# Kernel tuning notes

Hardware: AMD Instinct MI355X
Metric: run time of the kernel (lower is better)

## Reference

```python
import jax, jax.numpy as jnp
import numpy as np

N_NODES = 50000
N_EDGES = 800000
RATIO = 0.5


def setup_inputs() -> dict:
    key = jax.random.key(0)
    ks = jax.random.split(key, 10)
    x = jax.random.normal(ks[0], (N_NODES, 256), dtype=jnp.float32)
    edge_index = jax.random.randint(ks[1], (2, N_EDGES), 0, N_NODES, dtype=jnp.int32)
    edge_weight = jax.random.uniform(ks[2], (N_EDGES,), dtype=jnp.float32)
    sub_fea = jax.random.normal(ks[3], (1, 128), dtype=jnp.float32)
    W1 = jax.random.normal(ks[4], (256, 96), dtype=jnp.float32) * 0.05
    b1 = jax.random.normal(ks[5], (96,), dtype=jnp.float32) * 0.05
    W2 = jax.random.normal(ks[6], (96, 64), dtype=jnp.float32) * 0.05
    b2 = jax.random.normal(ks[7], (64,), dtype=jnp.float32) * 0.05
    fc_w = jax.random.normal(ks[8], (64, 128), dtype=jnp.float32) * 0.05
    fc_b = jax.random.normal(ks[9], (64,), dtype=jnp.float32) * 0.05
    return {"x": x, "edge_index": edge_index, "edge_weight": edge_weight,
            "sub_fea": sub_fea, "W1": W1, "b1": b1, "W2": W2, "b2": b2,
            "fc_w": fc_w, "fc_b": fc_b}


def reference(x, edge_index, edge_weight, sub_fea, W1, b1, W2, b2, fc_w, fc_b):
    N = x.shape[0]
    src, dst = edge_index[0], edge_index[1]

    def gcn_layer(h, W, b):
        # GraphConvolution: support = h @ W; out = spmm(adj, support) + b
        support = h @ W                              # [N, d_out]
        msgs = support[src] * edge_weight[:, None]   # gather + scale, [E, d_out]
        agg = jax.ops.segment_sum(msgs, dst, num_segments=N)  # scatter-add
        return agg + b

    h = jax.nn.relu(gcn_layer(x, W1, b1))            # [N, nhid]
    h = jax.nn.relu(gcn_layer(h, W2, b2))            # [N, nclass]
    # global_mean_pool(batch=None): mean over all nodes -> [1, nclass]
    pooled = jax.nn.selu(jnp.mean(h, axis=0, keepdims=True))
    # dropout in eval mode: identity
    x_ext = sub_fea @ fc_w.T + fc_b                  # [1, nclass]
    out = pooled + RATIO * x_ext
    return jax.nn.log_softmax(out, axis=1)
```

## Files before the change

### kernel.cpp

```cpp
#include <hip/hip_runtime.h>
#include <hip/hip_bf16.h>

#define N_NODES 50000
#define N_EDGES 800000
#define NBKT ((N_NODES + 127) / 128)
#define BCAP 4096

typedef __attribute__((ext_vector_type(8))) short short8;
typedef __attribute__((ext_vector_type(4))) float float4v;

__device__ __forceinline__ unsigned short f2bf(float f) {
    unsigned u = __float_as_uint(f);
    u += 0x7FFF + ((u >> 16) & 1);
    return (unsigned short)(u >> 16);
}
__device__ __forceinline__ float bf2f(unsigned short u) {
    return __uint_as_float((unsigned)u << 16);
}

__global__ __launch_bounds__(256) void prep_kernel(const float* __restrict__ W1,
                                                   const float* __restrict__ W2,
                                                   unsigned short* __restrict__ Wt1,
                                                   unsigned short* __restrict__ Wt2,
                                                   int* __restrict__ gcnt,
                                                   float* __restrict__ pooled) {
    int i = blockIdx.x * 256 + threadIdx.x;
    if (i < 24576) {
        int n = i >> 8, k = i & 255;
        Wt1[i] = f2bf(W1[k * 96 + n]);
    } else if (i < 30720) {
        int j = i - 24576;
        int n = j / 96, k = j - n * 96;
        Wt2[j] = f2bf(W2[k * 64 + n]);
    } else if (i < 30720 + NBKT) {
        gcnt[i - 30720] = 0;
    } else if (i < 30720 + NBKT + 64) {
        pooled[i - 30720 - NBKT] = 0.f;
    }
}

template <int K, int N, bool IN_BF16>
__global__ __launch_bounds__(256) void gemm_mfma_kernel(const void* __restrict__ src_,
                                                        const unsigned short* __restrict__ Wt,
                                                        unsigned short* __restrict__ outb) {
    constexpr int NF = N / 16;
    constexpr int LDA = 40;
    __shared__ unsigned short a_lds[64 * LDA];
    __shared__ unsigned short b_lds[N * LDA];
    const int tid = threadIdx.x;
    const int lane = tid & 63;
    const int w = tid >> 6;
    const int row0 = blockIdx.x * 64;
    const int fr = lane & 15;
    const int fk = (lane >> 4) * 8;

    float4v acc[NF];
    #pragma unroll
    for (int nn = 0; nn < NF; ++nn) acc[nn] = (float4v){0.f, 0.f, 0.f, 0.f};

    const int srow = tid >> 2;
    const int sko  = (tid & 3) * 8;

    for (int k0 = 0; k0 < K; k0 += 32) {
        {
            int grow = row0 + srow;
            short8 s = (short8){0, 0, 0, 0, 0, 0, 0, 0};
            if (grow < N_NODES) {
                if constexpr (IN_BF16) {
                    const unsigned short* src = (const unsigned short*)src_;
                    s = *reinterpret_cast<const short8*>(&src[(size_t)grow * K + k0 + sko]);
                } else {
                    const float* src = (const float*)src_;
                    const float4* p = reinterpret_cast<const float4*>(&src[(size_t)grow * K + k0 + sko]);
                    float4 v0 = p[0], v1 = p[1];
                    s[0] = (short)f2bf(v0.x); s[1] = (short)f2bf(v0.y);
                    s[2] = (short)f2bf(v0.z); s[3] = (short)f2bf(v0.w);
                    s[4] = (short)f2bf(v1.x); s[5] = (short)f2bf(v1.y);
                    s[6] = (short)f2bf(v1.z); s[7] = (short)f2bf(v1.w);
                }
            }
            *reinterpret_cast<short8*>(&a_lds[srow * LDA + sko]) = s;
        }
        for (int c = tid; c < N * 4; c += 256) {
            int n = c >> 2, ko = (c & 3) * 8;
            short8 s = *reinterpret_cast<const short8*>(&Wt[(size_t)n * K + k0 + ko]);
            *reinterpret_cast<short8*>(&b_lds[n * LDA + ko]) = s;
        }
        __syncthreads();
        short8 af = *reinterpret_cast<short8*>(&a_lds[(w * 16 + fr) * LDA + fk]);
        #pragma unroll
        for (int nn = 0; nn < NF; ++nn) {
            short8 bf = *reinterpret_cast<short8*>(&b_lds[(nn * 16 + fr) * LDA + fk]);
            acc[nn] = __builtin_amdgcn_mfma_f32_16x16x32_bf16(af, bf, acc[nn], 0, 0, 0);
        }
        __syncthreads();
    }
    const int orow_base = row0 + w * 16 + (lane >> 4) * 4;
    const int ocol = lane & 15;
    #pragma unroll
    for (int nn = 0; nn < NF; ++nn) {
        #pragma unroll
        for (int r = 0; r < 4; ++r) {
            int grow = orow_base + r;
            if (grow < N_NODES) outb[(size_t)grow * N + nn * 16 + ocol] = f2bf(acc[nn][r]);
        }
    }
}

__global__ __launch_bounds__(256) void bucket1_kernel(const int* __restrict__ srcv,
                                                      const int* __restrict__ dstv,
                                                      const float* __restrict__ wv,
                                                      int* __restrict__ gcnt,
                                                      int2* __restrict__ scratch) {
    __shared__ int lhist[NBKT];
    __shared__ int gb[NBKT];
    const int t = threadIdx.x;
    for (int i = t; i < NBKT; i += 256) lhist[i] = 0;
    __syncthreads();
    const int base = blockIdx.x * 4096;
    int rank[16], bkt[16], dst[16];
    unsigned pay[16];
    #pragma unroll
    for (int i = 0; i < 16; ++i) {
        int e = base + t + i * 256;
        if (e < N_EDGES) {
            int d = dstv[e];
            dst[i] = d;
            bkt[i] = d >> 7;
            unsigned w15 = __float2uint_rn(wv[e] * 32768.0f);
            if (w15 > 32767u) w15 = 32767u;
            pay[i] = ((unsigned)srcv[e] << 15) | w15;
            rank[i] = atomicAdd(&lhist[bkt[i]], 1);
        } else {
            bkt[i] = -1;
        }
    }
    __syncthreads();
    for (int b = t; b < NBKT; b += 256) {
        int c = lhist[b];
        gb[b] = (c > 0) ? atomicAdd(&gcnt[b], c) : 0;
    }
    __syncthreads();
    #pragma unroll
    for (int i = 0; i < 16; ++i) {
        if (bkt[i] >= 0) {
            int pos = gb[bkt[i]] + rank[i];
            if (pos < BCAP)
                scratch[(size_t)bkt[i] * BCAP + pos] = make_int2(dst[i], (int)pay[i]);
        }
    }
}

__global__ __launch_bounds__(512) void bscan_kernel(const int* __restrict__ gcnt,
                                                    int* __restrict__ bbase,
                                                    int* __restrict__ off) {
    __shared__ int sh[512];
    const int t = threadIdx.x;
    int v = (t < NBKT) ? min(gcnt[t], BCAP) : 0;
    sh[t] = v;
    __syncthreads();
    #pragma unroll
    for (int d = 1; d < 512; d <<= 1) {
        int u = (t >= d) ? sh[t - d] : 0;
        __syncthreads();
        sh[t] += u;
        __syncthreads();
    }
    if (t < NBKT) bbase[t] = sh[t] - v;
    if (t == NBKT - 1) off[N_NODES] = sh[t];
}

__global__ __launch_bounds__(256) void bucket2_kernel(const int2* __restrict__ scratch,
                                                      const int* __restrict__ gcnt,
                                                      const int* __restrict__ bbase,
                                                      int* __restrict__ off,
                                                      unsigned* __restrict__ ewq) {
    __shared__ int dh[128];
    __shared__ int sx[128];
    __shared__ int dcur[128];
    const int t = threadIdx.x;
    const int b = blockIdx.x;
    const int d0 = b << 7;
    const int cnt = min(gcnt[b], BCAP);
    const size_t sbase = (size_t)b * BCAP;
    const int obase = bbase[b];
    if (t < 128) dh[t] = 0;
    __syncthreads();
    for (int i = t; i < cnt; i += 256)
        atomicAdd(&dh[scratch[sbase + i].x & 127], 1);
    __syncthreads();
    int myc = (t < 128) ? dh[t] : 0;
    if (t < 128) sx[t] = myc;
    __syncthreads();
    #pragma unroll
    for (int d = 1; d < 128; d <<= 1) {
        int u = (t < 128 && t >= d) ? sx[t - d] : 0;
        __syncthreads();
        if (t < 128) sx[t] += u;
        __syncthreads();
    }
    if (t < 128) {
        int excl = obase + sx[t] - myc;
        dcur[t] = excl;
        if (d0 + t < N_NODES) off[d0 + t] = excl;
    }
    __syncthreads();
    for (int i = t; i < cnt; i += 256) {
        int2 e = scratch[sbase + i];
        int pos = atomicAdd(&dcur[e.x & 127], 1);
        ewq[pos] = (unsigned)e.y;
    }
}

template <int DIM, bool OUT_BF16>
__global__ __launch_bounds__(256) void gather_agg_kernel(const unsigned short* __restrict__ supb,
                                                         const int* __restrict__ off,
                                                         const unsigned* __restrict__ ewq,
                                                         const float* __restrict__ bias,
                                                         void* __restrict__ outp) {
    const int NQ = DIM / 4;
    const float kInv = 1.0f / 32768.0f;
    unsigned gid = blockIdx.x * 256u + threadIdx.x;
    if (gid >= (unsigned)N_NODES * NQ) return;
    unsigned n = gid / NQ;
    unsigned q = gid - n * NQ;
    const int e0 = off[n], e1 = off[n + 1];
    float4 acc[8];
    #pragma unroll
    for (int i = 0; i < 8; ++i) acc[i] = make_float4(0.f, 0.f, 0.f, 0.f);
    int e = e0;
    for (; e + 8 <= e1; e += 8) {
        unsigned p[8];
        #pragma unroll
        for (int i = 0; i < 8; ++i) p[i] = ewq[e + i];
        ushort4 u[8];
        #pragma unroll
        for (int i = 0; i < 8; ++i)
            u[i] = *reinterpret_cast<const ushort4*>(&supb[(size_t)(p[i] >> 15) * DIM + q * 4]);
        #pragma unroll
        for (int i = 0; i < 8; ++i) {
            float w = (float)(p[i] & 32767u) * kInv;
            acc[i].x += bf2f(u[i].x) * w;
            acc[i].y += bf2f(u[i].y) * w;
            acc[i].z += bf2f(u[i].z) * w;
            acc[i].w += bf2f(u[i].w) * w;
        }
    }
    for (; e < e1; ++e) {
        unsigned p = ewq[e];
        float w = (float)(p & 32767u) * kInv;
        ushort4 u = *reinterpret_cast<const ushort4*>(&supb[(size_t)(p >> 15) * DIM + q * 4]);
        acc[0].x += bf2f(u.x) * w;
        acc[0].y += bf2f(u.y) * w;
        acc[0].z += bf2f(u.z) * w;
        acc[0].w += bf2f(u.w) * w;
    }
    #pragma unroll
    for (int i = 1; i < 8; ++i) {
        acc[0].x += acc[i].x;
        acc[0].y += acc[i].y;
        acc[0].z += acc[i].z;
        acc[0].w += acc[i].w;
    }
    const float4 bb = *reinterpret_cast<const float4*>(&bias[q * 4]);
    float4 r;
    r.x = fmaxf(acc[0].x + bb.x, 0.f);
    r.y = fmaxf(acc[0].y + bb.y, 0.f);
    r.z = fmaxf(acc[0].z + bb.z, 0.f);
    r.w = fmaxf(acc[0].w + bb.w, 0.f);
    if (OUT_BF16) {
        ushort4 o;
        o.x = f2bf(r.x); o.y = f2bf(r.y); o.z = f2bf(r.z); o.w = f2bf(r.w);
        *reinterpret_cast<ushort4*>(&((unsigned short*)outp)[(size_t)n * DIM + q * 4]) = o;
    } else {
        *reinterpret_cast<float4*>(&((float*)outp)[(size_t)n * DIM + q * 4]) = r;
    }
}

__global__ __launch_bounds__(256) void colsum_kernel(const float* __restrict__ h2,
                                                     float* __restrict__ pooled) {
    __shared__ float red[4][64];
    const int t = threadIdx.x;
    const int c = t & 63, r = t >> 6;
    float s = 0.f;
    const int base = blockIdx.x * 256;
    for (int i = r; i < 256; i += 4) {
        int n = base + i;
        if (n < N_NODES) s += h2[(size_t)n * 64 + c];
    }
    red[r][c] = s;
    __syncthreads();
    if (r == 0) {
        float v = red[0][c] + red[1][c] + red[2][c] + red[3][c];
        unsafeAtomicAdd(&pooled[c], v);
    }
}

__global__ void final_kernel(const float* __restrict__ pooled,
                             const float* __restrict__ sub_fea,
                             const float* __restrict__ fc_w,
                             const float* __restrict__ fc_b,
                             float* __restrict__ out) {
    const int c = threadIdx.x;
    float p = pooled[c] * (1.0f / (float)N_NODES);
    const float kScale = 1.0507009873554805f;
    const float kAlpha = 1.6732632423543772f;
    float se = (p > 0.f) ? kScale * p : kScale * kAlpha * (expf(p) - 1.f);
    float xe = fc_b[c];
    for (int k = 0; k < 128; ++k) xe += sub_fea[k] * fc_w[c * 128 + k];
    float v = se + 0.5f * xe;
    float m = v;
    #pragma unroll
    for (int off = 32; off >= 1; off >>= 1) m = fmaxf(m, __shfl_xor(m, off));
    float ex = expf(v - m);
    float ss = ex;
    #pragma unroll
    for (int off = 32; off >= 1; off >>= 1) ss += __shfl_xor(ss, off);
    out[c] = v - m - logf(ss);
}

extern "C" void kernel_launch(void* const* d_in, const int* in_sizes, int n_in,
                              void* d_out, int out_size, void* d_ws, size_t ws_size,
                              hipStream_t stream) {
    const float* x       = (const float*)d_in[0];
    const int*   ei      = (const int*)d_in[1];
    const float* ew      = (const float*)d_in[2];
    const float* sub_fea = (const float*)d_in[3];
    const float* W1      = (const float*)d_in[4];
    const float* b1      = (const float*)d_in[5];
    const float* W2      = (const float*)d_in[6];
    const float* b2      = (const float*)d_in[7];
    const float* fc_w    = (const float*)d_in[8];
    const float* fc_b    = (const float*)d_in[9];
    float* out = (float*)d_out;

    char* base = (char*)d_ws;
    unsigned short* A   = (unsigned short*)(base);
    char*  Bb    = base + 9600000;
    float* pooled = (float*)(base + 22400000);
    int*   off   = (int*)(base + 22400512);
    int*   gcnt  = (int*)(base + 22600704);
    int*   bbase = (int*)(base + 22602752);
    unsigned* ewq = (unsigned*)(base + 22604800);
    int2*  scratch = (int2*)(base + 25804800);
    unsigned short* Wt1 = (unsigned short*)(base + 38617088);
    unsigned short* Wt2 = (unsigned short*)(base + 38666240);

    const int* srcv = ei;
    const int* dstv = ei + N_EDGES;

    prep_kernel<<<122, 256, 0, stream>>>(W1, W2, Wt1, Wt2, gcnt, pooled);

    bucket1_kernel<<<(N_EDGES + 4095) / 4096, 256, 0, stream>>>(srcv, dstv, ew, gcnt, scratch);
    bscan_kernel<<<1, 512, 0, stream>>>(gcnt, bbase, off);
    bucket2_kernel<<<NBKT, 256, 0, stream>>>(scratch, gcnt, bbase, off, ewq);

    gemm_mfma_kernel<256, 96, false><<<(N_NODES + 63) / 64, 256, 0, stream>>>(x, Wt1, A);
    {
        unsigned total = (unsigned)N_NODES * 24;
        gather_agg_kernel<96, true><<<(total + 255) / 256, 256, 0, stream>>>(
            A, off, ewq, b1, Bb);
    }

    gemm_mfma_kernel<96, 64, true><<<(N_NODES + 63) / 64, 256, 0, stream>>>(Bb, Wt2, A);
    {
        unsigned total = (unsigned)N_NODES * 16;
        gather_agg_kernel<64, false><<<(total + 255) / 256, 256, 0, stream>>>(
            A, off, ewq, b2, Bb);
    }

    colsum_kernel<<<(N_NODES + 255) / 256, 256, 0, stream>>>((const float*)Bb, pooled);
    final_kernel<<<1, 64, 0, stream>>>(pooled, sub_fea, fc_w, fc_b, out);
}
```

Before: 141.5 us.

## Fuse edge bucketing with first GEMM, drop scan kernel, store support in FP8

New measurement: 131.7 us. -6.9%, faster.

```diff
diff --git a/kernel.cpp b/kernel.cpp
--- a/kernel.cpp
+++ b/kernel.cpp
@@ -5,6 +5,8 @@
 #define N_EDGES 800000
 #define NBKT ((N_NODES + 127) / 128)
 #define BCAP 4096
+#define NB_B1 ((N_EDGES + 4095) / 4096)
+#define NB_GEMM1 ((N_NODES + 63) / 64)
 
 typedef __attribute__((ext_vector_type(8))) short short8;
 typedef __attribute__((ext_vector_type(4))) float float4v;
@@ -16,6 +18,19 @@
 }
 __device__ __forceinline__ float bf2f(unsigned short u) {
     return __uint_as_float((unsigned)u << 16);
+}
+__device__ __forceinline__ unsigned char f2fp8(float v) {
+    unsigned b = __float_as_uint(v * 0x1p-120f);
+    unsigned s = (b >> 24) & 0x80u;
+    unsigned mag = b & 0x7FFFFFFFu;
+    mag += 0x7FFFFu + ((mag >> 20) & 1u);
+    unsigned code = mag >> 20;
+    if (code > 0x7Eu) code = 0x7Eu;
+    return (unsigned char)(s | code);
+}
+__device__ __forceinline__ float fp82f(unsigned c) {
+    unsigned u = ((c & 0x80u) << 24) | ((c & 0x7Fu) << 20);
+    return __uint_as_float(u) * 0x1p+120f;
 }
 
 __global__ __launch_bounds__(256) void prep_kernel(const float* __restrict__ W1,
@@ -40,17 +55,17 @@
 }
 
 template <int K, int N, bool IN_BF16>
-__global__ __launch_bounds__(256) void gemm_mfma_kernel(const void* __restrict__ src_,
-                                                        const unsigned short* __restrict__ Wt,
-                                                        unsigned short* __restrict__ outb) {
+__device__ __forceinline__ void gemm_body(int bx, const void* __restrict__ src_,
+                                          const unsigned short* __restrict__ Wt,
+                                          unsigned char* __restrict__ outb,
+                                          unsigned short* a_lds,
+                                          unsigned short* b_lds) {
     constexpr int NF = N / 16;
     constexpr int LDA = 40;
-    __shared__ unsigned short a_lds[64 * LDA];
-    __shared__ unsigned short b_lds[N * LDA];
     const int tid = threadIdx.x;
     const int lane = tid & 63;
     const int w = tid >> 6;
-    const int row0 = blockIdx.x * 64;
+    const int row0 = bx * 64;
     const int fr = lane & 15;
     const int fk = (lane >> 4) * 8;
 
@@ -102,88 +117,96 @@
         #pragma unroll
         for (int r = 0; r < 4; ++r) {
             int grow = orow_base + r;
-            if (grow < N_NODES) outb[(size_t)grow * N + nn * 16 + ocol] = f2bf(acc[nn][r]);
-        }
-    }
-}
-
-__global__ __launch_bounds__(256) void bucket1_kernel(const int* __restrict__ srcv,
-                                                      const int* __restrict__ dstv,
-                                                      const float* __restrict__ wv,
-                                                      int* __restrict__ gcnt,
-                                                      int2* __restrict__ scratch) {
+            if (grow < N_NODES) outb[(size_t)grow * N + nn * 16 + ocol] = f2fp8(acc[nn][r]);
+        }
+    }
+}
+
+__global__ __launch_bounds__(256) void mega1_kernel(const int* __restrict__ srcv,
+                                                    const int* __restrict__ dstv,
+                                                    const float* __restrict__ wv,
+                                                    int* __restrict__ gcnt,
+                                                    int2* __restrict__ scratch,
+                                                    const float* __restrict__ x,
+                                                    const unsigned short* __restrict__ Wt1,
+                                                    unsigned char* __restrict__ outA) {
     __shared__ int lhist[NBKT];
     __shared__ int gb[NBKT];
+    __shared__ unsigned short a_lds[64 * 40];
+    __shared__ unsigned short b_lds[96 * 40];
     const int t = threadIdx.x;
-    for (int i = t; i < NBKT; i += 256) lhist[i] = 0;
-    __syncthreads();
-    const int base = blockIdx.x * 4096;
-    int rank[16], bkt[16], dst[16];
-    unsigned pay[16];
-    #pragma unroll
-    for (int i = 0; i < 16; ++i) {
-        int e = base + t + i * 256;
-        if (e < N_EDGES) {
-            int d = dstv[e];
-            dst[i] = d;
-            bkt[i] = d >> 7;
-            unsigned w15 = __float2uint_rn(wv[e] * 32768.0f);
-            if (w15 > 32767u) w15 = 32767u;
-            pay[i] = ((unsigned)srcv[e] << 15) | w15;
-            rank[i] = atomicAdd(&lhist[bkt[i]], 1);
-        } else {
-            bkt[i] = -1;
-        }
-    }
-    __syncthreads();
-    for (int b = t; b < NBKT; b += 256) {
-        int c = lhist[b];
-        gb[b] = (c > 0) ? atomicAdd(&gcnt[b], c) : 0;
-    }
-    __syncthreads();
-    #pragma unroll
-    for (int i = 0; i < 16; ++i) {
-        if (bkt[i] >= 0) {
-            int pos = gb[bkt[i]] + rank[i];
-            if (pos < BCAP)
-                scratch[(size_t)bkt[i] * BCAP + pos] = make_int2(dst[i], (int)pay[i]);
-        }
-    }
-}
-
-__global__ __launch_bounds__(512) void bscan_kernel(const int* __restrict__ gcnt,
-                                                    int* __restrict__ bbase,
-                                                    int* __restrict__ off) {
-    __shared__ int sh[512];
-    const int t = threadIdx.x;
-    int v = (t < NBKT) ? min(gcnt[t], BCAP) : 0;
-    sh[t] = v;
-    __syncthreads();
-    #pragma unroll
-    for (int d = 1; d < 512; d <<= 1) {
-        int u = (t >= d) ? sh[t - d] : 0;
-        __syncthreads();
-        sh[t] += u;
-        __syncthreads();
-    }
-    if (t < NBKT) bbase[t] = sh[t] - v;
-    if (t == NBKT - 1) off[N_NODES] = sh[t];
+    if (blockIdx.x < NB_B1) {
+        for (int i = t; i < NBKT; i += 256) lhist[i] = 0;
+        __syncthreads();
+        const int base = blockIdx.x * 4096;
+        int rank[16], bkt[16], dst[16];
+        unsigned pay[16];
+        #pragma unroll
+        for (int i = 0; i < 16; ++i) {
+            int e = base + t + i * 256;
+            if (e < N_EDGES) {
+                int d = dstv[e];
+                dst[i] = d;
+                bkt[i] = d >> 7;
+                unsigned w15 = __float2uint_rn(wv[e] * 32768.0f);
+                if (w15 > 32767u) w15 = 32767u;
+                pay[i] = ((unsigned)srcv[e] << 15) | w15;
+                rank[i] = atomicAdd(&lhist[bkt[i]], 1);
+            } else {
+                bkt[i] = -1;
+            }
+        }
+        __syncthreads();
+        for (int b = t; b < NBKT; b += 256) {
+            int c = lhist[b];
+            gb[b] = (c > 0) ? atomicAdd(&gcnt[b], c) : 0;
+        }
+        __syncthreads();
+        #pragma unroll
+        for (int i = 0; i < 16; ++i) {
+            if (bkt[i] >= 0) {
+                int pos = gb[bkt[i]] + rank[i];
+                if (pos < BCAP)
+                    scratch[(size_t)bkt[i] * BCAP + pos] = make_int2(dst[i], (int)pay[i]);
+            }
+        }
+    } else {
+        gemm_body<256, 96, false>(blockIdx.x - NB_B1, x, Wt1, outA, a_lds, b_lds);
+    }
+}
+
+__global__ __launch_bounds__(256) void gemm2_kernel(const unsigned short* __restrict__ h1,
+                                                    const unsigned short* __restrict__ Wt2,
+                                                    unsigned char* __restrict__ outA) {
+    __shared__ unsigned short a_lds[64 * 40];
+    __shared__ unsigned short b_lds[64 * 40];
+    gemm_body<96, 64, true>(blockIdx.x, h1, Wt2, outA, a_lds, b_lds);
 }
 
 __global__ __launch_bounds__(256) void bucket2_kernel(const int2* __restrict__ scratch,
                                                       const int* __restrict__ gcnt,
-                                                      const int* __restrict__ bbase,
                                                       int* __restrict__ off,
                                                       unsigned* __restrict__ ewq) {
     __shared__ int dh[128];
     __shared__ int sx[128];
     __shared__ int dcur[128];
+    __shared__ int redsum[256];
     const int t = threadIdx.x;
     const int b = blockIdx.x;
     const int d0 = b << 7;
     const int cnt = min(gcnt[b], BCAP);
     const size_t sbase = (size_t)b * BCAP;
-    const int obase = bbase[b];
+    int pre = 0;
+    for (int i = t; i < b; i += 256) pre += min(gcnt[i], BCAP);
+    redsum[t] = pre;
+    __syncthreads();
+    #pragma unroll
+    for (int d = 128; d > 0; d >>= 1) {
+        if (t < d) redsum[t] += redsum[t + d];
+        __syncthreads();
+    }
+    const int obase = redsum[0];
+    if (t == 0 && b == NBKT - 1) off[N_NODES] = obase + cnt;
     if (t < 128) dh[t] = 0;
     __syncthreads();
     for (int i = t; i < cnt; i += 256)
@@ -213,7 +236,7 @@
 }
 
 template <int DIM, bool OUT_BF16>
-__global__ __launch_bounds__(256) void gather_agg_kernel(const unsigned short* __restrict__ supb,
+__global__ __launch_bounds__(256) void gather_agg_kernel(const unsigned char* __restrict__ sup8,
                                                          const int* __restrict__ off,
                                                          const unsigned* __restrict__ ewq,
                                                          const float* __restrict__ bias,
@@ -233,27 +256,27 @@
         unsigned p[8];
         #pragma unroll
         for (int i = 0; i < 8; ++i) p[i] = ewq[e + i];
-        ushort4 u[8];
+        unsigned u[8];
         #pragma unroll
         for (int i = 0; i < 8; ++i)
-            u[i] = *reinterpret_cast<const ushort4*>(&supb[(size_t)(p[i] >> 15) * DIM + q * 4]);
+            u[i] = *reinterpret_cast<const unsigned*>(&sup8[(size_t)(p[i] >> 15) * DIM + q * 4]);
         #pragma unroll
         for (int i = 0; i < 8; ++i) {
             float w = (float)(p[i] & 32767u) * kInv;
-            acc[i].x += bf2f(u[i].x) * w;
-            acc[i].y += bf2f(u[i].y) * w;
-            acc[i].z += bf2f(u[i].z) * w;
-            acc[i].w += bf2f(u[i].w) * w;
+            acc[i].x += fp82f(u[i]) * w;
+            acc[i].y += fp82f(u[i] >> 8) * w;
+            acc[i].z += fp82f(u[i] >> 16) * w;
+            acc[i].w += fp82f(u[i] >> 24) * w;
         }
     }
     for (; e < e1; ++e) {
         unsigned p = ewq[e];
         float w = (float)(p & 32767u) * kInv;
-        ushort4 u = *reinterpret_cast<const ushort4*>(&supb[(size_t)(p >> 15) * DIM + q * 4]);
-        acc[0].x += bf2f(u.x) * w;
-        acc[0].y += bf2f(u.y) * w;
-        acc[0].z += bf2f(u.z) * w;
-        acc[0].w += bf2f(u.w) * w;
+        unsigned u = *reinterpret_cast<const unsigned*>(&sup8[(size_t)(p >> 15) * DIM + q * 4]);
+        acc[0].x += fp82f(u) * w;
+        acc[0].y += fp82f(u >> 8) * w;
+        acc[0].z += fp82f(u >> 16) * w;
+        acc[0].w += fp82f(u >> 24) * w;
     }
     #pragma unroll
     for (int i = 1; i < 8; ++i) {
@@ -335,38 +358,38 @@
     float* out = (float*)d_out;
 
     char* base = (char*)d_ws;
-    unsigned short* A   = (unsigned short*)(base);
-    char*  Bb    = base + 9600000;
-    float* pooled = (float*)(base + 22400000);
-    int*   off   = (int*)(base + 22400512);
-    int*   gcnt  = (int*)(base + 22600704);
-    int*   bbase = (int*)(base + 22602752);
-    unsigned* ewq = (unsigned*)(base + 22604800);
-    int2*  scratch = (int2*)(base + 25804800);
-    unsigned short* Wt1 = (unsigned short*)(base + 38617088);
-    unsigned short* Wt2 = (unsigned short*)(base + 38666240);
+    unsigned char* A = (unsigned char*)(base);
+    char*  Bb    = base + 4800000;
+    float* pooled = (float*)(base + 17600000);
+    int*   gcnt  = (int*)(base + 17600512);
+    int*   off   = (int*)(base + 17602560);
+    unsigned* ewq = (unsigned*)(base + 17802752);
+    int2*  scratch = (int2*)(base + 21002752);
+    unsigned short* Wt1 = (unsigned short*)(base + 33815040);
+    unsigned short* Wt2 = (unsigned short*)(base + 33864192);
 
     const int* srcv = ei;
     const int* dstv = ei + N_EDGES;
 
     prep_kernel<<<122, 256, 0, stream>>>(W1, W2, Wt1, Wt2, gcnt, pooled);
 
-    bucket1_kernel<<<(N_EDGES + 4095) / 4096, 256, 0, stream>>>(srcv, dstv, ew, gcnt, scratch);
-    bscan_kernel<<<1, 512, 0, stream>>>(gcnt, bbase, off);
-    bucket2_kernel<<<NBKT, 256, 0, stream>>>(scratch, gcnt, bbase, off, ewq);
-
-    gemm_mfma_kernel<256, 96, false><<<(N_NODES + 63) / 64, 256, 0, stream>>>(x, Wt1, A);
+    mega1_kernel<<<NB_B1 + NB_GEMM1, 256, 0, stream>>>(srcv, dstv, ew, gcnt, scratch,
+                                                       x, Wt1, A);
+
+    bucket2_kernel<<<NBKT, 256, 0, stream>>>(scratch, gcnt, off, ewq);
+
     {
         unsigned total = (unsigned)N_NODES * 24;
         gather_agg_kernel<96, true><<<(total + 255) / 256, 256, 0, stream>>>(
-            A, off, ewq, b1, Bb);
-    }
-
-    gemm_mfma_kernel<96, 64, true><<<(N_NODES + 63) / 64, 256, 0, stream>>>(Bb, Wt2, A);
+            A, off, ewq, b1, (void*)Bb);
+    }
+
+    gemm2_kernel<<<NB_GEMM1, 256, 0, stream>>>((const unsigned short*)Bb, Wt2, A);
+
     {
         unsigned total = (unsigned)N_NODES * 16;
         gather_agg_kernel<64, false><<<(total + 255) / 256, 256, 0, stream>>>(
-            A, off, ewq, b2, Bb);
+            A, off, ewq, b2, (void*)Bb);
     }
 
     colsum_kernel<<<(N_NODES + 255) / 256, 256, 0, stream>>>((const float*)Bb, pooled);
```
